# Kernel optimization log

Measured on AMD Instinct MI355X. Metric: run time of the kernel, lower is better.

Reference implementation:

```python
import jax, jax.numpy as jnp
import numpy as np

BS, ZDIM, HID, TLEN = 1024, 256, 256, 128


def setup_inputs() -> dict:
    key = jax.random.key(0)
    k1, k2, k3 = jax.random.split(key, 3)
    z0 = jax.random.normal(k1, (BS, ZDIM), dtype=jnp.float32)
    # strictly increasing time grid on [0, 1]
    t = jnp.linspace(0.0, 1.0, TLEN).astype(jnp.float32)
    # small init keeps the 127-step RK4 trajectory numerically stable
    W1 = jax.random.normal(k2, (ZDIM, HID), dtype=jnp.float32) * (0.5 / np.sqrt(ZDIM))
    b1 = jnp.zeros((HID,), dtype=jnp.float32)
    W2 = jax.random.normal(k3, (HID, ZDIM), dtype=jnp.float32) * (0.5 / np.sqrt(HID))
    b2 = jnp.zeros((ZDIM,), dtype=jnp.float32)
    return {"z0": z0, "t": t, "W1": W1, "b1": b1, "W2": W2, "b2": b2}


def reference(z0, t, W1, b1, W2, b2):
    # ODEF: f(z, t) = tanh(z @ W1 + b1) @ W2 + b2  (autonomous MLP dynamics)
    def f(z, ti):
        return jnp.tanh(z @ W1 + b1) @ W2 + b2

    def rk4_step(z, ts):
        t0, t1 = ts
        h = t1 - t0
        k1 = f(z, t0)
        k2 = f(z + k1 * (h * 0.5), t0 + h * 0.5)
        k3 = f(z + k2 * (h * 0.5), t0 + h * 0.5)
        k4 = f(z + k3 * h, t0 + h)
        zn = z + (h / 6.0) * (k1 + 2.0 * k2 + 2.0 * k3 + k4)
        return zn, None
    # sequential integration over time_len-1 intervals (matches the python loop)
    zT, _ = jax.lax.scan(rk4_step, z0, (t[:-1], t[1:]))
    # NeuralODE.forward default: return_whole_sequence=False -> z[-1]
    return zT
```

## Files before the change

### kernel.cpp

```cpp
#include <hip/hip_runtime.h>
#include <hip/hip_bf16.h>


#define BS   1024
#define ZDIM 256
#define TLEN 128
#define ROWSTRIDE 264

typedef short v8s __attribute__((ext_vector_type(8)));
typedef float v4f __attribute__((ext_vector_type(4)));

static __device__ __forceinline__ ushort f2bf_rne(float x) {
    union { float f; unsigned u; } v; v.f = x;
    unsigned r = v.u + 0x7FFFu + ((v.u >> 16) & 1u);
    return (ushort)(r >> 16);
}

static __device__ __forceinline__ unsigned pk2(float a, float b) {
    union { __hip_bfloat162 h; unsigned u; } cv;
    cv.h = __float22bfloat162_rn(make_float2(a, b));
    return cv.u;
}

static __device__ __forceinline__ float fast_tanh(float x) {
    float e = __builtin_amdgcn_exp2f(2.88539008177793f * x);
    float r = __builtin_amdgcn_rcpf(e + 1.0f);
    return 1.0f - 2.0f * r;
}

__global__ __launch_bounds__(512, 2)
void ode_mfma_kernel(const float* __restrict__ z0,
                     const float* __restrict__ t,
                     const float* __restrict__ W1,
                     const float* __restrict__ b1,
                     const float* __restrict__ W2,
                     const float* __restrict__ b2,
                     float* __restrict__ out)
{
    __shared__ ushort zbuf[16 * ROWSTRIDE];
    __shared__ ushort hbuf[16 * ROWSTRIDE];
    __shared__ float  hsh[TLEN];

    const int tid  = threadIdx.x;
    const int wv   = tid >> 6;
    const int lane = tid & 63;
    const int q    = lane >> 4;
    const int ln   = lane & 15;
    const int rowbase = blockIdx.x * 16;

    if (tid < TLEN - 1) hsh[tid] = t[tid + 1] - t[tid];

    v8s w1f[2][8], w2f[2][8];
    #pragma unroll
    for (int ct = 0; ct < 2; ++ct) {
        const int c = wv * 32 + ct * 16 + ln;
        #pragma unroll
        for (int i = 0; i < 8; ++i) {
            const int ks = (wv + i) & 7;
            v8s a, b;
            #pragma unroll
            for (int j = 0; j < 8; ++j) {
                const int k = ks * 32 + q * 8 + j;
                a[j] = (short)f2bf_rne(W1[k * ZDIM + c]);
                b[j] = (short)f2bf_rne(W2[k * ZDIM + c]);
            }
            w1f[ct][i] = a;
            w2f[ct][i] = b;
        }
    }

    v4f b1f[2], b2f[2];
    #pragma unroll
    for (int ct = 0; ct < 2; ++ct)
        #pragma unroll
        for (int r = 0; r < 4; ++r) {
            b1f[ct][r] = b1[wv * 32 + ct * 16 + q * 4 + r];
            b2f[ct][r] = b2[wv * 32 + ct * 16 + q * 4 + r];
        }

    const int rdbase = ln * ROWSTRIDE + q * 8;
    const int wrbase = ln * ROWSTRIDE + wv * 32 + q * 4;
    int rdaddr[8];
    #pragma unroll
    for (int i = 0; i < 8; ++i)
        rdaddr[i] = rdbase + ((wv + i) & 7) * 32;

    float zloc[2][4];
    #pragma unroll
    for (int ct = 0; ct < 2; ++ct) {
        #pragma unroll
        for (int r = 0; r < 4; ++r)
            zloc[ct][r] = z0[(rowbase + ln) * ZDIM + wv * 32 + ct * 16 + q * 4 + r];
        uint2 p; p.x = pk2(zloc[ct][0], zloc[ct][1]); p.y = pk2(zloc[ct][2], zloc[ct][3]);
        *(uint2*)&zbuf[wrbase + ct * 16] = p;
    }
    __syncthreads();

    float kacc[2][4];

    #pragma unroll 1
    for (int step = 0; step < TLEN - 1; ++step) {
        const float h = hsh[step];

        #pragma unroll
        for (int stage = 0; stage < 4; ++stage) {
            v4f acc0 = b1f[0], acc1 = b1f[1];
            #pragma unroll
            for (int i = 0; i < 8; ++i) {
                const v8s zf = *(const v8s*)&zbuf[rdaddr[i]];
                acc0 = __builtin_amdgcn_mfma_f32_16x16x32_bf16(w1f[0][i], zf, acc0, 0, 0, 0);
                acc1 = __builtin_amdgcn_mfma_f32_16x16x32_bf16(w1f[1][i], zf, acc1, 0, 0, 0);
            }
            {
                uint2 p0;
                p0.x = pk2(fast_tanh(acc0[0]), fast_tanh(acc0[1]));
                p0.y = pk2(fast_tanh(acc0[2]), fast_tanh(acc0[3]));
                *(uint2*)&hbuf[wrbase] = p0;
                uint2 p1;
                p1.x = pk2(fast_tanh(acc1[0]), fast_tanh(acc1[1]));
                p1.y = pk2(fast_tanh(acc1[2]), fast_tanh(acc1[3]));
                *(uint2*)&hbuf[wrbase + 16] = p1;
            }
            __syncthreads();

            v4f fv0 = b2f[0], fv1 = b2f[1];
            #pragma unroll
            for (int i = 0; i < 8; ++i) {
                const v8s hf = *(const v8s*)&hbuf[rdaddr[i]];
                fv0 = __builtin_amdgcn_mfma_f32_16x16x32_bf16(w2f[0][i], hf, fv0, 0, 0, 0);
                fv1 = __builtin_amdgcn_mfma_f32_16x16x32_bf16(w2f[1][i], hf, fv1, 0, 0, 0);
            }

            if (stage < 3) {
                const float c = (stage == 2) ? h : 0.5f * h;
                #pragma unroll
                for (int ct = 0; ct < 2; ++ct) {
                    const v4f f = ct ? fv1 : fv0;
                    float zn[4];
                    #pragma unroll
                    for (int r = 0; r < 4; ++r) zn[r] = zloc[ct][r] + c * f[r];
                    uint2 p; p.x = pk2(zn[0], zn[1]); p.y = pk2(zn[2], zn[3]);
                    *(uint2*)&zbuf[wrbase + ct * 16] = p;
                }
                __syncthreads();
                #pragma unroll
                for (int ct = 0; ct < 2; ++ct) {
                    const v4f f = ct ? fv1 : fv0;
                    #pragma unroll
                    for (int r = 0; r < 4; ++r) {
                        if (stage == 0) kacc[ct][r] = f[r];
                        else            kacc[ct][r] += 2.0f * f[r];
                    }
                }
            } else {
                #pragma unroll
                for (int ct = 0; ct < 2; ++ct) {
                    const v4f f = ct ? fv1 : fv0;
                    #pragma unroll
                    for (int r = 0; r < 4; ++r) {
                        kacc[ct][r] += f[r];
                        zloc[ct][r] += (h * (1.0f / 6.0f)) * kacc[ct][r];
                    }
                    uint2 p; p.x = pk2(zloc[ct][0], zloc[ct][1]);
                    p.y = pk2(zloc[ct][2], zloc[ct][3]);
                    *(uint2*)&zbuf[wrbase + ct * 16] = p;
                }
                __syncthreads();
            }
        }
    }

    #pragma unroll
    for (int ct = 0; ct < 2; ++ct)
        #pragma unroll
        for (int r = 0; r < 4; ++r)
            out[(rowbase + ln) * ZDIM + wv * 32 + ct * 16 + q * 4 + r] = zloc[ct][r];
}

extern "C" void kernel_launch(void* const* d_in, const int* in_sizes, int n_in,
                              void* d_out, int out_size, void* d_ws, size_t ws_size,
                              hipStream_t stream) {
    const float* z0 = (const float*)d_in[0];
    const float* t  = (const float*)d_in[1];
    const float* W1 = (const float*)d_in[2];
    const float* b1 = (const float*)d_in[3];
    const float* W2 = (const float*)d_in[4];
    const float* b2 = (const float*)d_in[5];
    float* out = (float*)d_out;

    dim3 grid(BS / 16);
    dim3 block(512);
    hipLaunchKernelGGL(ode_mfma_kernel, grid, block, 0, stream,
                       z0, t, W1, b1, W2, b2, out);
}
```

Measured before the change: 546.3 us.

## Use 4 waves per block with 64 columns each instead of 8 waves

Halves the block to 256 threads, and each wave now owns 64 output columns (4 MFMA tiles) instead of 32. It keeps twice as many bf16 weight fragments in registers. The aim is fewer waves contending at each of the per-stage barriers and more independent MFMA chains per wave to hide latency. In exchange each wave's register footprint doubles (128 v8s weight fragments), with a risk of spills or lower occupancy, and with only 64 blocks on the device fewer waves are active overall.

```diff
diff --git a/kernel.cpp b/kernel.cpp
--- a/kernel.cpp
+++ b/kernel.cpp
@@ -28,7 +28,7 @@
     return 1.0f - 2.0f * r;
 }
 
-__global__ __launch_bounds__(512, 2)
+__global__ __launch_bounds__(256, 1)
 void ode_mfma_kernel(const float* __restrict__ z0,
                      const float* __restrict__ t,
                      const float* __restrict__ W1,
@@ -50,13 +50,13 @@
 
     if (tid < TLEN - 1) hsh[tid] = t[tid + 1] - t[tid];
 
-    v8s w1f[2][8], w2f[2][8];
-    #pragma unroll
-    for (int ct = 0; ct < 2; ++ct) {
-        const int c = wv * 32 + ct * 16 + ln;
+    v8s w1f[4][8], w2f[4][8];
+    #pragma unroll
+    for (int ct = 0; ct < 4; ++ct) {
+        const int c = wv * 64 + ct * 16 + ln;
         #pragma unroll
         for (int i = 0; i < 8; ++i) {
-            const int ks = (wv + i) & 7;
+            const int ks = (2 * wv + i) & 7;
             v8s a, b;
             #pragma unroll
             for (int j = 0; j < 8; ++j) {
@@ -69,34 +69,34 @@
         }
     }
 
-    v4f b1f[2], b2f[2];
-    #pragma unroll
-    for (int ct = 0; ct < 2; ++ct)
+    v4f b1f[4], b2f[4];
+    #pragma unroll
+    for (int ct = 0; ct < 4; ++ct)
         #pragma unroll
         for (int r = 0; r < 4; ++r) {
-            b1f[ct][r] = b1[wv * 32 + ct * 16 + q * 4 + r];
-            b2f[ct][r] = b2[wv * 32 + ct * 16 + q * 4 + r];
+            b1f[ct][r] = b1[wv * 64 + ct * 16 + q * 4 + r];
+            b2f[ct][r] = b2[wv * 64 + ct * 16 + q * 4 + r];
         }
 
     const int rdbase = ln * ROWSTRIDE + q * 8;
-    const int wrbase = ln * ROWSTRIDE + wv * 32 + q * 4;
+    const int wrbase = ln * ROWSTRIDE + wv * 64 + q * 4;
     int rdaddr[8];
     #pragma unroll
     for (int i = 0; i < 8; ++i)
-        rdaddr[i] = rdbase + ((wv + i) & 7) * 32;
-
-    float zloc[2][4];
-    #pragma unroll
-    for (int ct = 0; ct < 2; ++ct) {
+        rdaddr[i] = rdbase + ((2 * wv + i) & 7) * 32;
+
+    float zloc[4][4];
+    #pragma unroll
+    for (int ct = 0; ct < 4; ++ct) {
         #pragma unroll
         for (int r = 0; r < 4; ++r)
-            zloc[ct][r] = z0[(rowbase + ln) * ZDIM + wv * 32 + ct * 16 + q * 4 + r];
+            zloc[ct][r] = z0[(rowbase + ln) * ZDIM + wv * 64 + ct * 16 + q * 4 + r];
         uint2 p; p.x = pk2(zloc[ct][0], zloc[ct][1]); p.y = pk2(zloc[ct][2], zloc[ct][3]);
         *(uint2*)&zbuf[wrbase + ct * 16] = p;
     }
     __syncthreads();
 
-    float kacc[2][4];
+    float kacc[4][4];
 
     #pragma unroll 1
     for (int step = 0; step < TLEN - 1; ++step) {
@@ -104,61 +104,67 @@
 
         #pragma unroll
         for (int stage = 0; stage < 4; ++stage) {
-            v4f acc0 = b1f[0], acc1 = b1f[1];
+            v4f a0 = b1f[0], a1 = b1f[1], a2 = b1f[2], a3 = b1f[3];
             #pragma unroll
             for (int i = 0; i < 8; ++i) {
                 const v8s zf = *(const v8s*)&zbuf[rdaddr[i]];
-                acc0 = __builtin_amdgcn_mfma_f32_16x16x32_bf16(w1f[0][i], zf, acc0, 0, 0, 0);
-                acc1 = __builtin_amdgcn_mfma_f32_16x16x32_bf16(w1f[1][i], zf, acc1, 0, 0, 0);
+                a0 = __builtin_amdgcn_mfma_f32_16x16x32_bf16(w1f[0][i], zf, a0, 0, 0, 0);
+                a1 = __builtin_amdgcn_mfma_f32_16x16x32_bf16(w1f[1][i], zf, a1, 0, 0, 0);
+                a2 = __builtin_amdgcn_mfma_f32_16x16x32_bf16(w1f[2][i], zf, a2, 0, 0, 0);
+                a3 = __builtin_amdgcn_mfma_f32_16x16x32_bf16(w1f[3][i], zf, a3, 0, 0, 0);
             }
             {
-                uint2 p0;
-                p0.x = pk2(fast_tanh(acc0[0]), fast_tanh(acc0[1]));
-                p0.y = pk2(fast_tanh(acc0[2]), fast_tanh(acc0[3]));
-                *(uint2*)&hbuf[wrbase] = p0;
-                uint2 p1;
-                p1.x = pk2(fast_tanh(acc1[0]), fast_tanh(acc1[1]));
-                p1.y = pk2(fast_tanh(acc1[2]), fast_tanh(acc1[3]));
-                *(uint2*)&hbuf[wrbase + 16] = p1;
+                uint2 p;
+                p.x = pk2(fast_tanh(a0[0]), fast_tanh(a0[1]));
+                p.y = pk2(fast_tanh(a0[2]), fast_tanh(a0[3]));
+                *(uint2*)&hbuf[wrbase] = p;
+                p.x = pk2(fast_tanh(a1[0]), fast_tanh(a1[1]));
+                p.y = pk2(fast_tanh(a1[2]), fast_tanh(a1[3]));
+                *(uint2*)&hbuf[wrbase + 16] = p;
+                p.x = pk2(fast_tanh(a2[0]), fast_tanh(a2[1]));
+                p.y = pk2(fast_tanh(a2[2]), fast_tanh(a2[3]));
+                *(uint2*)&hbuf[wrbase + 32] = p;
+                p.x = pk2(fast_tanh(a3[0]), fast_tanh(a3[1]));
+                p.y = pk2(fast_tanh(a3[2]), fast_tanh(a3[3]));
+                *(uint2*)&hbuf[wrbase + 48] = p;
             }
             __syncthreads();
 
-            v4f fv0 = b2f[0], fv1 = b2f[1];
+            v4f f0 = b2f[0], f1 = b2f[1], f2 = b2f[2], f3 = b2f[3];
             #pragma unroll
             for (int i = 0; i < 8; ++i) {
                 const v8s hf = *(const v8s*)&hbuf[rdaddr[i]];
-                fv0 = __builtin_amdgcn_mfma_f32_16x16x32_bf16(w2f[0][i], hf, fv0, 0, 0, 0);
-                fv1 = __builtin_amdgcn_mfma_f32_16x16x32_bf16(w2f[1][i], hf, fv1, 0, 0, 0);
-            }
+                f0 = __builtin_amdgcn_mfma_f32_16x16x32_bf16(w2f[0][i], hf, f0, 0, 0, 0);
+                f1 = __builtin_amdgcn_mfma_f32_16x16x32_bf16(w2f[1][i], hf, f1, 0, 0, 0);
+                f2 = __builtin_amdgcn_mfma_f32_16x16x32_bf16(w2f[2][i], hf, f2, 0, 0, 0);
+                f3 = __builtin_amdgcn_mfma_f32_16x16x32_bf16(w2f[3][i], hf, f3, 0, 0, 0);
+            }
+            v4f fa[4] = { f0, f1, f2, f3 };
 
             if (stage < 3) {
                 const float c = (stage == 2) ? h : 0.5f * h;
                 #pragma unroll
-                for (int ct = 0; ct < 2; ++ct) {
-                    const v4f f = ct ? fv1 : fv0;
+                for (int ct = 0; ct < 4; ++ct) {
                     float zn[4];
                     #pragma unroll
-                    for (int r = 0; r < 4; ++r) zn[r] = zloc[ct][r] + c * f[r];
+                    for (int r = 0; r < 4; ++r) zn[r] = zloc[ct][r] + c * fa[ct][r];
                     uint2 p; p.x = pk2(zn[0], zn[1]); p.y = pk2(zn[2], zn[3]);
                     *(uint2*)&zbuf[wrbase + ct * 16] = p;
                 }
                 __syncthreads();
                 #pragma unroll
-                for (int ct = 0; ct < 2; ++ct) {
-                    const v4f f = ct ? fv1 : fv0;
+                for (int ct = 0; ct < 4; ++ct)
                     #pragma unroll
                     for (int r = 0; r < 4; ++r) {
-                        if (stage == 0) kacc[ct][r] = f[r];
-                        else            kacc[ct][r] += 2.0f * f[r];
+                        if (stage == 0) kacc[ct][r] = fa[ct][r];
+                        else            kacc[ct][r] += 2.0f * fa[ct][r];
                     }
-                }
             } else {
                 #pragma unroll
-                for (int ct = 0; ct < 2; ++ct) {
-                    const v4f f = ct ? fv1 : fv0;
+                for (int ct = 0; ct < 4; ++ct) {
                     #pragma unroll
                     for (int r = 0; r < 4; ++r) {
-                        kacc[ct][r] += f[r];
+                        kacc[ct][r] += fa[ct][r];
                         zloc[ct][r] += (h * (1.0f / 6.0f)) * kacc[ct][r];
                     }
                     uint2 p; p.x = pk2(zloc[ct][0], zloc[ct][1]);
@@ -171,10 +177,10 @@
     }
 
     #pragma unroll
-    for (int ct = 0; ct < 2; ++ct)
+    for (int ct = 0; ct < 4; ++ct)
         #pragma unroll
         for (int r = 0; r < 4; ++r)
-            out[(rowbase + ln) * ZDIM + wv * 32 + ct * 16 + q * 4 + r] = zloc[ct][r];
+            out[(rowbase + ln) * ZDIM + wv * 64 + ct * 16 + q * 4 + r] = zloc[ct][r];
 }
 
 extern "C" void kernel_launch(void* const* d_in, const int* in_sizes, int n_in,
@@ -189,7 +195,7 @@
     float* out = (float*)d_out;
 
     dim3 grid(BS / 16);
-    dim3 block(512);
+    dim3 block(256);
     hipLaunchKernelGGL(ode_mfma_kernel, grid, block, 0, stream,
                        z0, t, W1, b1, W2, b2, out);
 }
```

After: 706.9 us. +29.4%, slower.

## Halve rows per block to double grid size and spread work across more CUs

Applied to the files above, without the earlier changes.

Each block now handles 8 batch rows instead of 16, which doubles the grid from 64 to 128 blocks. The MFMA tiles stay 16 wide, so lanes 8-15 duplicate rows 0-7 and their shared-memory and global writes are masked off. The goal is to put more of the GPU's compute units to work, since 64 blocks leave most CUs idle during the long sequential RK4 loop. In exchange, half of the MFMA work in each block is redundant, and every block repeats the weight load and bf16 conversion.

```diff
diff --git a/kernel.cpp b/kernel.cpp
--- a/kernel.cpp
+++ b/kernel.cpp
@@ -5,6 +5,7 @@
 #define BS   1024
 #define ZDIM 256
 #define TLEN 128
+#define ROWS 8
 #define ROWSTRIDE 264
 
 typedef short v8s __attribute__((ext_vector_type(8)));
@@ -37,8 +38,8 @@
                      const float* __restrict__ b2,
                      float* __restrict__ out)
 {
-    __shared__ ushort zbuf[16 * ROWSTRIDE];
-    __shared__ ushort hbuf[16 * ROWSTRIDE];
+    __shared__ ushort zbuf[ROWS * ROWSTRIDE];
+    __shared__ ushort hbuf[ROWS * ROWSTRIDE];
     __shared__ float  hsh[TLEN];
 
     const int tid  = threadIdx.x;
@@ -46,7 +47,8 @@
     const int lane = tid & 63;
     const int q    = lane >> 4;
     const int ln   = lane & 15;
-    const int rowbase = blockIdx.x * 16;
+    const int mr   = ln & 7;
+    const int rowbase = blockIdx.x * ROWS;
 
     if (tid < TLEN - 1) hsh[tid] = t[tid + 1] - t[tid];
 
@@ -78,8 +80,8 @@
             b2f[ct][r] = b2[wv * 32 + ct * 16 + q * 4 + r];
         }
 
-    const int rdbase = ln * ROWSTRIDE + q * 8;
-    const int wrbase = ln * ROWSTRIDE + wv * 32 + q * 4;
+    const int rdbase = mr * ROWSTRIDE + q * 8;
+    const int wrbase = mr * ROWSTRIDE + wv * 32 + q * 4;
     int rdaddr[8];
     #pragma unroll
     for (int i = 0; i < 8; ++i)
@@ -90,9 +92,11 @@
     for (int ct = 0; ct < 2; ++ct) {
         #pragma unroll
         for (int r = 0; r < 4; ++r)
-            zloc[ct][r] = z0[(rowbase + ln) * ZDIM + wv * 32 + ct * 16 + q * 4 + r];
-        uint2 p; p.x = pk2(zloc[ct][0], zloc[ct][1]); p.y = pk2(zloc[ct][2], zloc[ct][3]);
-        *(uint2*)&zbuf[wrbase + ct * 16] = p;
+            zloc[ct][r] = z0[(rowbase + mr) * ZDIM + wv * 32 + ct * 16 + q * 4 + r];
+        if (ln < 8) {
+            uint2 p; p.x = pk2(zloc[ct][0], zloc[ct][1]); p.y = pk2(zloc[ct][2], zloc[ct][3]);
+            *(uint2*)&zbuf[wrbase + ct * 16] = p;
+        }
     }
     __syncthreads();
 
@@ -115,11 +119,11 @@
                 uint2 p0;
                 p0.x = pk2(fast_tanh(acc0[0]), fast_tanh(acc0[1]));
                 p0.y = pk2(fast_tanh(acc0[2]), fast_tanh(acc0[3]));
-                *(uint2*)&hbuf[wrbase] = p0;
+                if (ln < 8) *(uint2*)&hbuf[wrbase] = p0;
                 uint2 p1;
                 p1.x = pk2(fast_tanh(acc1[0]), fast_tanh(acc1[1]));
                 p1.y = pk2(fast_tanh(acc1[2]), fast_tanh(acc1[3]));
-                *(uint2*)&hbuf[wrbase + 16] = p1;
+                if (ln < 8) *(uint2*)&hbuf[wrbase + 16] = p1;
             }
             __syncthreads();
 
@@ -139,8 +143,10 @@
                     float zn[4];
                     #pragma unroll
                     for (int r = 0; r < 4; ++r) zn[r] = zloc[ct][r] + c * f[r];
-                    uint2 p; p.x = pk2(zn[0], zn[1]); p.y = pk2(zn[2], zn[3]);
-                    *(uint2*)&zbuf[wrbase + ct * 16] = p;
+                    if (ln < 8) {
+                        uint2 p; p.x = pk2(zn[0], zn[1]); p.y = pk2(zn[2], zn[3]);
+                        *(uint2*)&zbuf[wrbase + ct * 16] = p;
+                    }
                 }
                 __syncthreads();
                 #pragma unroll
@@ -161,20 +167,24 @@
                         kacc[ct][r] += f[r];
                         zloc[ct][r] += (h * (1.0f / 6.0f)) * kacc[ct][r];
                     }
-                    uint2 p; p.x = pk2(zloc[ct][0], zloc[ct][1]);
-                    p.y = pk2(zloc[ct][2], zloc[ct][3]);
-                    *(uint2*)&zbuf[wrbase + ct * 16] = p;
+                    if (ln < 8) {
+                        uint2 p; p.x = pk2(zloc[ct][0], zloc[ct][1]);
+                        p.y = pk2(zloc[ct][2], zloc[ct][3]);
+                        *(uint2*)&zbuf[wrbase + ct * 16] = p;
+                    }
                 }
                 __syncthreads();
             }
         }
     }
 
-    #pragma unroll
-    for (int ct = 0; ct < 2; ++ct)
-        #pragma unroll
-        for (int r = 0; r < 4; ++r)
-            out[(rowbase + ln) * ZDIM + wv * 32 + ct * 16 + q * 4 + r] = zloc[ct][r];
+    if (ln < 8) {
+        #pragma unroll
+        for (int ct = 0; ct < 2; ++ct)
+            #pragma unroll
+            for (int r = 0; r < 4; ++r)
+                out[(rowbase + mr) * ZDIM + wv * 32 + ct * 16 + q * 4 + r] = zloc[ct][r];
+    }
 }
 
 extern "C" void kernel_launch(void* const* d_in, const int* in_sizes, int n_in,
@@ -188,7 +198,7 @@
     const float* b2 = (const float*)d_in[5];
     float* out = (float*)d_out;
 
-    dim3 grid(BS / 16);
+    dim3 grid(BS / ROWS);
     dim3 block(512);
     hipLaunchKernelGGL(ode_mfma_kernel, grid, block, 0, stream,
                        z0, t, W1, b1, W2, b2, out);
```

Result: slower. 582.1 us (+6.6%).

## Replace block barriers with LDS counter spin-waits and double-buffer z

Applied to the files above, without the earlier changes.

Swaps each __syncthreads in the RK4 stage loop for a shared-memory atomic counter. Each wave bumps the counter after its LDS writes and spins, with s_sleep, until the counter reaches a per-stage stamp. The z staging buffer is split into two ping-pong buffers so a wave can write the next stage input while slower waves may still be reading the current one. The aim is to loosen lock-step barrier synchronisation between the 8 waves. In exchange it adds atomic and spin-poll latency, and it relies on a bounded spin that silently breaks out after a timeout.

```diff
diff --git a/kernel.cpp b/kernel.cpp
--- a/kernel.cpp
+++ b/kernel.cpp
@@ -27,6 +27,20 @@
     float r = __builtin_amdgcn_rcpf(e + 1.0f);
     return 1.0f - 2.0f * r;
 }
+
+#define SPIN_GE(cptr, stamp) do {                                   \
+    int _g = 0;                                                     \
+    while (*(volatile int*)(cptr) < (stamp)) {                      \
+        __builtin_amdgcn_s_sleep(1);                                \
+        if (++_g > (1 << 17)) break;                                \
+    }                                                               \
+    __builtin_amdgcn_sched_barrier(0);                              \
+} while (0)
+
+#define FLAG_ADD(cptr, lanev) do {                                  \
+    asm volatile("s_waitcnt lgkmcnt(0)" ::: "memory");              \
+    if ((lanev) == 0) atomicAdd((cptr), 1);                         \
+} while (0)
 
 __global__ __launch_bounds__(512, 2)
 void ode_mfma_kernel(const float* __restrict__ z0,
@@ -37,9 +51,11 @@
                      const float* __restrict__ b2,
                      float* __restrict__ out)
 {
-    __shared__ ushort zbuf[16 * ROWSTRIDE];
-    __shared__ ushort hbuf[16 * ROWSTRIDE];
+    __shared__ ushort zbufA[16 * ROWSTRIDE];
+    __shared__ ushort zbufB[16 * ROWSTRIDE];
+    __shared__ ushort hbuf [16 * ROWSTRIDE];
     __shared__ float  hsh[TLEN];
+    __shared__ int    zcnt, hcnt;
 
     const int tid  = threadIdx.x;
     const int wv   = tid >> 6;
@@ -48,6 +64,7 @@
     const int ln   = lane & 15;
     const int rowbase = blockIdx.x * 16;
 
+    if (tid == 0) { zcnt = 8; hcnt = 0; }
     if (tid < TLEN - 1) hsh[tid] = t[tid + 1] - t[tid];
 
     v8s w1f[2][8], w2f[2][8];
@@ -92,7 +109,7 @@
         for (int r = 0; r < 4; ++r)
             zloc[ct][r] = z0[(rowbase + ln) * ZDIM + wv * 32 + ct * 16 + q * 4 + r];
         uint2 p; p.x = pk2(zloc[ct][0], zloc[ct][1]); p.y = pk2(zloc[ct][2], zloc[ct][3]);
-        *(uint2*)&zbuf[wrbase + ct * 16] = p;
+        *(uint2*)&zbufA[wrbase + ct * 16] = p;
     }
     __syncthreads();
 
@@ -101,13 +118,19 @@
     #pragma unroll 1
     for (int step = 0; step < TLEN - 1; ++step) {
         const float h = hsh[step];
+        const int stampbase = step * 32;
 
         #pragma unroll
         for (int stage = 0; stage < 4; ++stage) {
+            const int stamp = stampbase + stage * 8 + 8;
+            ushort* const zr = (stage & 1) ? zbufB : zbufA;
+            ushort* const zw = (stage & 1) ? zbufA : zbufB;
+
+            SPIN_GE(&zcnt, stamp);
             v4f acc0 = b1f[0], acc1 = b1f[1];
             #pragma unroll
             for (int i = 0; i < 8; ++i) {
-                const v8s zf = *(const v8s*)&zbuf[rdaddr[i]];
+                const v8s zf = *(const v8s*)&zr[rdaddr[i]];
                 acc0 = __builtin_amdgcn_mfma_f32_16x16x32_bf16(w1f[0][i], zf, acc0, 0, 0, 0);
                 acc1 = __builtin_amdgcn_mfma_f32_16x16x32_bf16(w1f[1][i], zf, acc1, 0, 0, 0);
             }
@@ -121,8 +144,9 @@
                 p1.y = pk2(fast_tanh(acc1[2]), fast_tanh(acc1[3]));
                 *(uint2*)&hbuf[wrbase + 16] = p1;
             }
-            __syncthreads();
-
+            FLAG_ADD(&hcnt, lane);
+
+            SPIN_GE(&hcnt, stamp);
             v4f fv0 = b2f[0], fv1 = b2f[1];
             #pragma unroll
             for (int i = 0; i < 8; ++i) {
@@ -140,9 +164,9 @@
                     #pragma unroll
                     for (int r = 0; r < 4; ++r) zn[r] = zloc[ct][r] + c * f[r];
                     uint2 p; p.x = pk2(zn[0], zn[1]); p.y = pk2(zn[2], zn[3]);
-                    *(uint2*)&zbuf[wrbase + ct * 16] = p;
+                    *(uint2*)&zw[wrbase + ct * 16] = p;
                 }
-                __syncthreads();
+                FLAG_ADD(&zcnt, lane);
                 #pragma unroll
                 for (int ct = 0; ct < 2; ++ct) {
                     const v4f f = ct ? fv1 : fv0;
@@ -163,9 +187,9 @@
                     }
                     uint2 p; p.x = pk2(zloc[ct][0], zloc[ct][1]);
                     p.y = pk2(zloc[ct][2], zloc[ct][3]);
-                    *(uint2*)&zbuf[wrbase + ct * 16] = p;
+                    *(uint2*)&zw[wrbase + ct * 16] = p;
                 }
-                __syncthreads();
+                FLAG_ADD(&zcnt, lane);
             }
         }
     }
```

New measurement: 707.0 us. 29.4% more time.
